# Performance work log

Measured on AMD Instinct MI355X. Metric: run time of the kernel, lower is better.

Reference implementation:

```python
import jax, jax.numpy as jnp
import numpy as np
from jax import lax

B, CIN, VS, P, E, H = 1, 1, 64, 4, 64, 8
N = (VS // P) ** 3  # 4096 patches
OUT = CIN * P ** 3  # 64
SCALE = 1.0 / float(np.sqrt(E))
EPS = 1e-5


def setup_inputs() -> dict:
    key = jax.random.key(0)
    ks = jax.random.split(key, 8)
    sc = 0.02
    return {
        "voxel": jax.random.normal(ks[0], (B, CIN, VS, VS, VS), jnp.float32),
        "conv_w": jax.random.normal(ks[1], (E, CIN, P, P, P), jnp.float32) * sc,
        "conv_b": jnp.zeros((E,), jnp.float32),
        "ln_g": jnp.ones((E,), jnp.float32),
        "ln_b": jnp.zeros((E,), jnp.float32),
        "pos_emb": jax.random.normal(ks[2], (1, N, E), jnp.float32) * sc,
        "wqk": jax.random.normal(ks[3], (E, H * E), jnp.float32) * sc,
        "bqk": jnp.zeros((H * E,), jnp.float32),
        "wv": jax.random.normal(ks[4], (E, H * E), jnp.float32) * sc,
        "bv": jnp.zeros((H * E,), jnp.float32),
        "alpha": jnp.array(1.0, jnp.float32),
        "wout": jax.random.normal(ks[5], (H * E, OUT), jnp.float32) * sc,
        "bout": jnp.zeros((OUT,), jnp.float32),
    }


def reference(voxel, conv_w, conv_b, ln_g, ln_b, pos_emb, wqk, bqk, wv, bv, alpha, wout, bout):
    # VoxelPatchEmbedding: strided Conv3d -> flatten -> permute -> LayerNorm
    emb = lax.conv_general_dilated(
        voxel, conv_w, window_strides=(P, P, P), padding="VALID",
        dimension_numbers=("NCDHW", "OIDHW", "NCDHW"))
    emb = emb + conv_b[None, :, None, None, None]
    b = emb.shape[0]
    emb = emb.reshape(b, E, -1).transpose(0, 2, 1)  # [B, N, E]
    mu = jnp.mean(emb, axis=-1, keepdims=True)
    var = jnp.var(emb, axis=-1, keepdims=True)
    emb = (emb - mu) * lax.rsqrt(var + EPS) * ln_g + ln_b
    emb = emb + pos_emb

    # tied Q/K projection; heads to dim 1: [B, H, N, E]
    qk_proj = (emb @ wqk + bqk).reshape(b, -1, H, E).transpose(0, 2, 1, 3)
    q = qk_proj
    k = qk_proj
    v = (emb @ wv + bv).reshape(b, -1, H, E).transpose(0, 2, 1, 3)

    # L2 distance: q^2 + k^2 - 2 q.k^T  -> [B, H, N, N]
    q2 = jnp.sum(q * q, axis=-1, keepdims=True)           # [B,H,N,1]
    k2 = jnp.sum(k * k, axis=-1, keepdims=True)           # [B,H,N,1]
    dist = q2 + k2.transpose(0, 1, 3, 2) - 2.0 * jnp.einsum("bhnd,bhmd->bhnm", q, k)

    scores = alpha * jnp.exp(-dist) * SCALE
    attn_w = jax.nn.softmax(scores, axis=-1)
    attn = jnp.einsum("bhnm,bhmd->bhnd", attn_w, v)       # [B,H,N,E]
    attn = attn.transpose(0, 2, 1, 3).reshape(b, -1, H * E)
    return attn @ wout + bout                              # [B, N, CIN*P^3]
```

## Files before the change

### kernel.cpp

```cpp
#include <hip/hip_runtime.h>
#include <hip/hip_bf16.h>

#define NPAT 4096
#define EDIM 64
#define NH   8
#define HE   512
#define OUTD 64

typedef short bf16x8 __attribute__((ext_vector_type(8)));
typedef float f32x4  __attribute__((ext_vector_type(4)));
typedef unsigned short u16x4 __attribute__((ext_vector_type(4)));

#if __has_builtin(__builtin_amdgcn_exp2f)
#define EXP2(x) __builtin_amdgcn_exp2f(x)
#else
#define EXP2(x) exp2f(x)
#endif

__device__ __forceinline__ ushort f2bf(float f) {
    uint u = __builtin_bit_cast(uint, f);
    return (ushort)((u + 0x7FFFu + ((u >> 16) & 1u)) >> 16);
}
__device__ __forceinline__ float bf2f(ushort b) {
    return __builtin_bit_cast(float, ((uint)b) << 16);
}

__global__ __launch_bounds__(256) void k_embed(
    const float* __restrict__ voxel,
    const float* __restrict__ conv_w,
    const float* __restrict__ conv_b,
    const float* __restrict__ ln_g, const float* __restrict__ ln_b,
    const float* __restrict__ pos,
    float* __restrict__ emb)
{
    const int b = blockIdx.x;
    const int d = b >> 6, hh = (b >> 2) & 15, wq = b & 3;
    const int t = threadIdx.x;
    __shared__ float wsm[64][68];
    __shared__ float vox[4][64];

    for (int i = t; i < 4096; i += 256) wsm[i >> 6][i & 63] = conv_w[i];
    {
        const int pair = t >> 4;
        const int q16  = t & 15;
        const float v = voxel[(d * 4 + (pair >> 2)) * 4096 + (hh * 4 + (pair & 3)) * 64 +
                              wq * 16 + q16];
        vox[q16 >> 2][pair * 4 + (q16 & 3)] = v;
    }
    __syncthreads();

    const int p = t >> 6;
    const int e = t & 63;
    const int n = d * 256 + hh * 16 + wq * 4 + p;

    float acc = conv_b[e];
    #pragma unroll
    for (int mi = 0; mi < 16; mi++) {
        const float4 vv = *(const float4*)&vox[p][mi * 4];
        const float4 ww = *(const float4*)&wsm[e][mi * 4];
        acc += vv.x * ww.x + vv.y * ww.y + vv.z * ww.z + vv.w * ww.w;
    }

    float s1 = acc, s2 = acc * acc;
    #pragma unroll
    for (int off = 1; off < 64; off <<= 1) {
        s1 += __shfl_xor(s1, off);
        s2 += __shfl_xor(s2, off);
    }
    const float mu  = s1 * (1.0f / 64.0f);
    const float var = s2 * (1.0f / 64.0f) - mu * mu;
    emb[n * 64 + e] = (acc - mu) * rsqrtf(var + 1e-5f) * ln_g[e] + ln_b[e] + pos[n * 64 + e];
}

__global__ __launch_bounds__(256) void k_wt(
    const float* __restrict__ wout,
    ushort* __restrict__ woutT)
{
    const int b = blockIdx.x;
    const int t = threadIdx.x;
    __shared__ float ld[64][65];
    for (int i = t; i < 4096; i += 256) ld[i >> 6][i & 63] = wout[(b * 64 + (i >> 6)) * 64 + (i & 63)];
    __syncthreads();
    const int o = t >> 2, kb = (t & 3) * 16;
    #pragma unroll
    for (int j = 0; j < 16; j++)
        woutT[o * 512 + b * 64 + kb + j] = f2bf(ld[kb + j][o]);
}

__global__ __launch_bounds__(256) void k_proj(
    const float* __restrict__ emb,
    const float* __restrict__ wqk, const float* __restrict__ bqk,
    const float* __restrict__ wv,  const float* __restrict__ bvv,
    ushort* __restrict__ qk_bf,
    ushort* __restrict__ vT_bf,
    float* __restrict__ q2)
{
    const int n0 = blockIdx.x * 16;
    const int h  = blockIdx.y;
    const int t  = threadIdx.x;
    const int e  = t & 63, rg = t >> 6;
    __shared__ float es[16][64];
    for (int i = t; i < 1024; i += 256) es[i >> 6][i & 63] = emb[n0 * 64 + i];
    __syncthreads();

    const int he = h * 64 + e;
    const float bq = bqk[he], bv = bvv[he];
    float aq[4] = {bq, bq, bq, bq};
    float av[4] = {bv, bv, bv, bv};

    for (int ep = 0; ep < 64; ep++) {
        const float wq = wqk[ep * HE + he];
        const float wvv = wv[ep * HE + he];
        #pragma unroll
        for (int rr = 0; rr < 4; rr++) {
            const float x = es[rg * 4 + rr][ep];
            aq[rr] += x * wq;
            av[rr] += x * wvv;
        }
    }

    u16x4 vpk;
    #pragma unroll
    for (int rr = 0; rr < 4; rr++) {
        const int n = n0 + rg * 4 + rr;
        const ushort qb = f2bf(aq[rr]);
        qk_bf[((size_t)h * NPAT + n) * 64 + e] = qb;
        const float qf = bf2f(qb);
        float s = qf * qf;
        #pragma unroll
        for (int off = 1; off < 64; off <<= 1) s += __shfl_xor(s, off);
        if (e == 0) q2[h * NPAT + n] = s;
        vpk[rr] = f2bf(av[rr]);
    }
    *(u16x4*)&vT_bf[((size_t)h * 64 + e) * NPAT + n0 + rg * 4] = vpk;
}

__global__ __launch_bounds__(1024, 8) void k_attn(
    const ushort* __restrict__ qk,
    const ushort* __restrict__ vT,
    const float* __restrict__ q2,
    const float* __restrict__ alpha,
    ushort* __restrict__ attn)
{
    const int bid = blockIdx.x;
    const int h  = bid & 7;
    const int bx = bid >> 3;
    const int tid = threadIdx.x;
    const int w  = tid >> 6;
    const int u  = w & 3;
    const int rg = w >> 2;
    const int l  = tid & 63;
    const int lr = l & 15;
    const int lg = l >> 4;
    const float L2E = 1.4426950408889634f;
    const float ccl2e = alpha[0] * 0.125f * L2E;

    __shared__ ushort kv_lds[2][2][64 * 64];
    __shared__ ushort p_lds[4][16 * 64];
    __shared__ float  zpart[4][4][16];

    const ushort* qkh = qk + (size_t)h * NPAT * 64;
    const ushort* vTh = vT + (size_t)h * 64 * NPAT;
    const float*  q2h = q2 + h * NPAT;

    const int row0 = bx * 64 + rg * 16;

    bf16x8 aq0, aq1;
    {
        const ushort* qrow = qkh + (size_t)(row0 + lr) * 64 + 8 * lg;
        aq0 = *(const bf16x8*)(qrow);
        aq1 = *(const bf16x8*)(qrow + 32);
    }
    float nq2[4];
    #pragma unroll
    for (int r = 0; r < 4; r++) nq2[r] = q2h[row0 + 4 * lg + r];

    const int w8   = w & 7;
    const int srow = w8 * 8 + (l >> 3);
    const int sch  = (l & 7) ^ (srow & 7);
    const ushort* ksrc0 = qkh + (size_t)srow * 64 + sch * 8;
    const ushort* vsrc0 = vTh + (size_t)srow * NPAT + sch * 8;
#define STAGE(bufi, it)                                                          \
    do {                                                                         \
        const ushort* _src = (w < 8) ? (ksrc0 + (size_t)(it) * 4096)             \
                                     : (vsrc0 + (size_t)(it) * 64);              \
        ushort* _dst = &kv_lds[bufi][w >> 3][w8 * 512];                          \
        __builtin_amdgcn_global_load_lds(                                        \
            (const __attribute__((address_space(1))) unsigned int*)_src,         \
            (__attribute__((address_space(3))) unsigned int*)_dst, 16, 0, 0);    \
    } while (0)

    f32x4 acc = (f32x4){0.f, 0.f, 0.f, 0.f};
    float zacc[4] = {0.f, 0.f, 0.f, 0.f};

    const int x7 = (lr & 7);
    char* prg = (char*)&p_lds[rg][0];

    STAGE(0, 0);
    float k2c = q2h[u * 16 + lr];

    for (int it = 0; it < 64; ++it) {
        const int buf = it & 1;
        __syncthreads();
        if (it + 1 < 64) STAGE(buf ^ 1, it + 1);
        float k2n = (it + 1 < 64) ? q2h[(it + 1) * 64 + u * 16 + lr] : 0.f;

        {
            const ushort* kb = &kv_lds[buf][0][0];
            const int krow = u * 16 + lr;
            bf16x8 bk0 = *(const bf16x8*)(kb + krow * 64 + ((lg ^ x7) << 3));
            bf16x8 bk1 = *(const bf16x8*)(kb + krow * 64 + (((lg + 4) ^ x7) << 3));
            f32x4 sc = (f32x4){0.f, 0.f, 0.f, 0.f};
            sc = __builtin_amdgcn_mfma_f32_16x16x32_bf16(aq0, bk0, sc, 0, 0, 0);
            sc = __builtin_amdgcn_mfma_f32_16x16x32_bf16(aq1, bk1, sc, 0, 0, 0);
            #pragma unroll
            for (int r = 0; r < 4; r++) {
                const float d = nq2[r] + k2c - 2.0f * sc[r];
                const float p = EXP2(ccl2e * EXP2(-L2E * d));
                zacc[r] += p;
                const int prow = 4 * lg + r, pcol = 16 * u + lr;
                const int byteoff = prow * 128 + ((pcol * 2) ^ ((prow & 7) << 4));
                *(ushort*)(prg + byteoff) = f2bf(p);
            }
        }
        asm volatile("s_waitcnt lgkmcnt(0)" ::: "memory");
        __builtin_amdgcn_s_barrier();

        {
            const ushort* vb = &kv_lds[buf][1][0];
            const int vrow = u * 16 + lr;
            bf16x8 bv0 = *(const bf16x8*)(vb + vrow * 64 + ((lg ^ x7) << 3));
            bf16x8 bv1 = *(const bf16x8*)(vb + vrow * 64 + (((lg + 4) ^ x7) << 3));
            char* rb = prg + lr * 128;
            const int xx = x7 << 4;
            bf16x8 pa0 = *(const bf16x8*)(rb + ((16 * lg) ^ xx));
            bf16x8 pa1 = *(const bf16x8*)(rb + ((64 + 16 * lg) ^ xx));
            acc = __builtin_amdgcn_mfma_f32_16x16x32_bf16(pa0, bv0, acc, 0, 0, 0);
            acc = __builtin_amdgcn_mfma_f32_16x16x32_bf16(pa1, bv1, acc, 0, 0, 0);
        }
        k2c = k2n;
    }
#undef STAGE

    #pragma unroll
    for (int r = 0; r < 4; r++) {
        float z = zacc[r];
        z += __shfl_xor(z, 1); z += __shfl_xor(z, 2);
        z += __shfl_xor(z, 4); z += __shfl_xor(z, 8);
        if (lr == 0) zpart[rg][u][4 * lg + r] = z;
    }
    __syncthreads();
    #pragma unroll
    for (int r = 0; r < 4; r++) {
        const int row = 4 * lg + r;
        const float zt = zpart[rg][0][row] + zpart[rg][1][row] +
                         zpart[rg][2][row] + zpart[rg][3][row];
        attn[(size_t)(row0 + row) * HE + h * 64 + u * 16 + lr] = f2bf(acc[r] / zt);
    }
}

__global__ __launch_bounds__(256) void k_out(
    const ushort* __restrict__ attn,
    const ushort* __restrict__ woutT,
    const float* __restrict__ bout,
    float* __restrict__ out)
{
    const int n0 = blockIdx.x * 8;
    const int t = threadIdx.x;
    const int w = t >> 6, l = t & 63, lr = l & 15, lg = l >> 4;
    __shared__ ushort sa[8][520];

    for (int c = t; c < 512; c += 256) {
        const int row = c >> 6, c8 = c & 63;
        *(bf16x8*)&sa[row][c8 * 8] = *(const bf16x8*)&attn[(size_t)(n0 + row) * 512 + c8 * 8];
    }
    __syncthreads();

    f32x4 acc = (f32x4){0.f, 0.f, 0.f, 0.f};
    const ushort* bp = woutT + (size_t)(w * 16 + lr) * 512 + 8 * lg;
    #pragma unroll
    for (int kk = 0; kk < 16; kk++) {
        bf16x8 a = *(const bf16x8*)&sa[lr & 7][kk * 32 + 8 * lg];
        bf16x8 bb = *(const bf16x8*)(bp + kk * 32);
        acc = __builtin_amdgcn_mfma_f32_16x16x32_bf16(a, bb, acc, 0, 0, 0);
    }
    if (lg < 2) {
        const float bo = bout[w * 16 + lr];
        #pragma unroll
        for (int r = 0; r < 4; r++)
            out[(size_t)(n0 + 4 * lg + r) * 64 + w * 16 + lr] = acc[r] + bo;
    }
}

extern "C" void kernel_launch(void* const* d_in, const int* in_sizes, int n_in,
                              void* d_out, int out_size, void* d_ws, size_t ws_size,
                              hipStream_t stream) {
    (void)in_sizes; (void)n_in; (void)out_size; (void)ws_size;
    const float* voxel  = (const float*)d_in[0];
    const float* conv_w = (const float*)d_in[1];
    const float* conv_b = (const float*)d_in[2];
    const float* ln_g   = (const float*)d_in[3];
    const float* ln_b   = (const float*)d_in[4];
    const float* pos    = (const float*)d_in[5];
    const float* wqk    = (const float*)d_in[6];
    const float* bqk    = (const float*)d_in[7];
    const float* wv     = (const float*)d_in[8];
    const float* bvv    = (const float*)d_in[9];
    const float* alpha  = (const float*)d_in[10];
    const float* wout   = (const float*)d_in[11];
    const float* bout   = (const float*)d_in[12];
    float* out = (float*)d_out;

    char* ws = (char*)d_ws;
    float*  emb     = (float*) (ws);
    ushort* qk_bf   = (ushort*)(ws + (1u << 20));
    ushort* vT_bf   = (ushort*)(ws + 5u * (1u << 20));
    float*  q2      = (float*) (ws + 9u * (1u << 20));
    ushort* attn_bf = (ushort*)(ws + 9u * (1u << 20) + (128u << 10));
    ushort* woutT   = (ushort*)(ws + 13u * (1u << 20) + (128u << 10));

    k_embed<<<1024, 256, 0, stream>>>(voxel, conv_w, conv_b, ln_g, ln_b, pos, emb);
    k_wt<<<8, 256, 0, stream>>>(wout, woutT);
    k_proj<<<dim3(NPAT / 16, NH), 256, 0, stream>>>(emb, wqk, bqk, wv, bvv, qk_bf, vT_bf, q2);
    k_attn<<<NPAT / 64 * NH, 1024, 0, stream>>>(qk_bf, vT_bf, q2, alpha, attn_bf);
    k_out<<<NPAT / 8, 256, 0, stream>>>(attn_bf, woutT, bout, out);
}
```

Baseline: 202.1 us.

## Fuse embed, weight transpose and projection; triple-buffer attention K/V staging

Merges the patch-embedding conv+LayerNorm, the output-weight transpose and the QK/V projection into one launch. Each projection block now recomputes the embedding for its 16 patches, so the fp32 emb buffer is never written out or read back. The attention kernel moves from double to triple buffering of K/V tiles in LDS, with vmcnt-based waits in place of a full sync each iteration. It also preloads all per-head k2 norms into shared memory instead of reading them from global each step. The cost is that the conv and LayerNorm work is repeated once per head (8x) and LDS use per attention block goes up.

Result: slower. 220.1 us (+8.9%).

```diff
diff --git a/kernel.cpp b/kernel.cpp
--- a/kernel.cpp
+++ b/kernel.cpp
@@ -25,82 +25,77 @@
     return __builtin_bit_cast(float, ((uint)b) << 16);
 }
 
-__global__ __launch_bounds__(256) void k_embed(
-    const float* __restrict__ voxel,
-    const float* __restrict__ conv_w,
-    const float* __restrict__ conv_b,
-    const float* __restrict__ ln_g, const float* __restrict__ ln_b,
-    const float* __restrict__ pos,
-    float* __restrict__ emb)
+__global__ __launch_bounds__(256) void k_embproj(
+    const float* __restrict__ voxel, const float* __restrict__ conv_w,
+    const float* __restrict__ conv_b, const float* __restrict__ ln_g,
+    const float* __restrict__ ln_b, const float* __restrict__ pos,
+    const float* __restrict__ wqk, const float* __restrict__ bqk,
+    const float* __restrict__ wv, const float* __restrict__ bvv,
+    const float* __restrict__ wout,
+    ushort* __restrict__ qk_bf,
+    ushort* __restrict__ vT_bf,
+    float* __restrict__ q2,
+    ushort* __restrict__ woutT)
 {
-    const int b = blockIdx.x;
-    const int d = b >> 6, hh = (b >> 2) & 15, wq = b & 3;
+    __shared__ float smem[64 * 65 + 16 * 64 + 16 * 64];
+    float (*wsm)[65] = (float(*)[65])smem;
+    float (*vox)[64] = (float(*)[64])(smem + 64 * 65);
+    float (*es)[64]  = (float(*)[64])(smem + 64 * 65 + 16 * 64);
     const int t = threadIdx.x;
-    __shared__ float wsm[64][68];
-    __shared__ float vox[4][64];
+
+    if (blockIdx.y == 8) {
+        if (blockIdx.x >= 8) return;
+        const int b = blockIdx.x;
+        for (int i = t; i < 4096; i += 256)
+            wsm[i >> 6][i & 63] = wout[(b * 64 + (i >> 6)) * 64 + (i & 63)];
+        __syncthreads();
+        const int o = t >> 2, kb = (t & 3) * 16;
+        #pragma unroll
+        for (int j = 0; j < 16; j++)
+            woutT[o * 512 + b * 64 + kb + j] = f2bf(wsm[kb + j][o]);
+        return;
+    }
+
+    const int bx = blockIdx.x, h = blockIdx.y;
+    const int n0 = bx * 16;
+    const int d = bx >> 4, hh = bx & 15;
+    const int e = t & 63, rg = t >> 6;
 
     for (int i = t; i < 4096; i += 256) wsm[i >> 6][i & 63] = conv_w[i];
     {
         const int pair = t >> 4;
-        const int q16  = t & 15;
-        const float v = voxel[(d * 4 + (pair >> 2)) * 4096 + (hh * 4 + (pair & 3)) * 64 +
-                              wq * 16 + q16];
-        vox[q16 >> 2][pair * 4 + (q16 & 3)] = v;
-    }
-    __syncthreads();
-
-    const int p = t >> 6;
-    const int e = t & 63;
-    const int n = d * 256 + hh * 16 + wq * 4 + p;
-
-    float acc = conv_b[e];
-    #pragma unroll
-    for (int mi = 0; mi < 16; mi++) {
-        const float4 vv = *(const float4*)&vox[p][mi * 4];
-        const float4 ww = *(const float4*)&wsm[e][mi * 4];
-        acc += vv.x * ww.x + vv.y * ww.y + vv.z * ww.z + vv.w * ww.w;
-    }
-
-    float s1 = acc, s2 = acc * acc;
-    #pragma unroll
-    for (int off = 1; off < 64; off <<= 1) {
-        s1 += __shfl_xor(s1, off);
-        s2 += __shfl_xor(s2, off);
-    }
-    const float mu  = s1 * (1.0f / 64.0f);
-    const float var = s2 * (1.0f / 64.0f) - mu * mu;
-    emb[n * 64 + e] = (acc - mu) * rsqrtf(var + 1e-5f) * ln_g[e] + ln_b[e] + pos[n * 64 + e];
-}
-
-__global__ __launch_bounds__(256) void k_wt(
-    const float* __restrict__ wout,
-    ushort* __restrict__ woutT)
-{
-    const int b = blockIdx.x;
-    const int t = threadIdx.x;
-    __shared__ float ld[64][65];
-    for (int i = t; i < 4096; i += 256) ld[i >> 6][i & 63] = wout[(b * 64 + (i >> 6)) * 64 + (i & 63)];
-    __syncthreads();
-    const int o = t >> 2, kb = (t & 3) * 16;
-    #pragma unroll
-    for (int j = 0; j < 16; j++)
-        woutT[o * 512 + b * 64 + kb + j] = f2bf(ld[kb + j][o]);
-}
-
-__global__ __launch_bounds__(256) void k_proj(
-    const float* __restrict__ emb,
-    const float* __restrict__ wqk, const float* __restrict__ bqk,
-    const float* __restrict__ wv,  const float* __restrict__ bvv,
-    ushort* __restrict__ qk_bf,
-    ushort* __restrict__ vT_bf,
-    float* __restrict__ q2)
-{
-    const int n0 = blockIdx.x * 16;
-    const int h  = blockIdx.y;
-    const int t  = threadIdx.x;
-    const int e  = t & 63, rg = t >> 6;
-    __shared__ float es[16][64];
-    for (int i = t; i < 1024; i += 256) es[i >> 6][i & 63] = emb[n0 * 64 + i];
+        const int off4 = (t & 15) * 4;
+        const float4 v = *(const float4*)&voxel[(d * 4 + (pair >> 2)) * 4096 +
+                                                (hh * 4 + (pair & 3)) * 64 + off4];
+        *(float4*)&vox[pair][off4] = v;
+    }
+    __syncthreads();
+
+    {
+        float acc[4];
+        #pragma unroll
+        for (int rr = 0; rr < 4; rr++) acc[rr] = conv_b[e];
+        for (int m = 0; m < 64; m++) {
+            const float wm = wsm[e][m];
+            #pragma unroll
+            for (int rr = 0; rr < 4; rr++)
+                acc[rr] += vox[m >> 2][(rg * 4 + rr) * 4 + (m & 3)] * wm;
+        }
+        #pragma unroll
+        for (int rr = 0; rr < 4; rr++) {
+            const int row = rg * 4 + rr;
+            float s1 = acc[rr], s2 = acc[rr] * acc[rr];
+            #pragma unroll
+            for (int off = 1; off < 64; off <<= 1) {
+                s1 += __shfl_xor(s1, off);
+                s2 += __shfl_xor(s2, off);
+            }
+            const float mu  = s1 * (1.0f / 64.0f);
+            const float var = s2 * (1.0f / 64.0f) - mu * mu;
+            es[row][e] = (acc[rr] - mu) * rsqrtf(var + 1e-5f) * ln_g[e] + ln_b[e] +
+                         pos[(n0 + row) * 64 + e];
+        }
+    }
     __syncthreads();
 
     const int he = h * 64 + e;
@@ -109,7 +104,7 @@
     float av[4] = {bv, bv, bv, bv};
 
     for (int ep = 0; ep < 64; ep++) {
-        const float wq = wqk[ep * HE + he];
+        const float wq  = wqk[ep * HE + he];
         const float wvv = wv[ep * HE + he];
         #pragma unroll
         for (int rr = 0; rr < 4; rr++) {
@@ -155,9 +150,10 @@
     const float L2E = 1.4426950408889634f;
     const float ccl2e = alpha[0] * 0.125f * L2E;
 
-    __shared__ ushort kv_lds[2][2][64 * 64];
+    __shared__ ushort kv_lds[3][2][64 * 64];
     __shared__ ushort p_lds[4][16 * 64];
     __shared__ float  zpart[4][4][16];
+    __shared__ float  q2s[4096];
 
     const ushort* qkh = qk + (size_t)h * NPAT * 64;
     const ushort* vTh = vT + (size_t)h * 64 * NPAT;
@@ -174,6 +170,8 @@
     float nq2[4];
     #pragma unroll
     for (int r = 0; r < 4; r++) nq2[r] = q2h[row0 + 4 * lg + r];
+
+    *(float4*)&q2s[tid * 4] = *(const float4*)&q2h[tid * 4];
 
     const int w8   = w & 7;
     const int srow = w8 * 8 + (l >> 3);
@@ -197,13 +195,19 @@
     char* prg = (char*)&p_lds[rg][0];
 
     STAGE(0, 0);
-    float k2c = q2h[u * 16 + lr];
-
+    STAGE(1, 1);
+    __syncthreads();
+
+    int buf = 0;
     for (int it = 0; it < 64; ++it) {
-        const int buf = it & 1;
-        __syncthreads();
-        if (it + 1 < 64) STAGE(buf ^ 1, it + 1);
-        float k2n = (it + 1 < 64) ? q2h[(it + 1) * 64 + u * 16 + lr] : 0.f;
+        if (it == 63) { asm volatile("s_waitcnt vmcnt(0)" ::: "memory"); }
+        else         { asm volatile("s_waitcnt vmcnt(1)" ::: "memory"); }
+        __builtin_amdgcn_s_barrier();
+        if (it + 2 < 64) {
+            int b2 = buf + 2; if (b2 >= 3) b2 -= 3;
+            STAGE(b2, it + 2);
+        }
+        const float k2c = q2s[it * 64 + u * 16 + lr];
 
         {
             const ushort* kb = &kv_lds[buf][0][0];
@@ -238,7 +242,7 @@
             acc = __builtin_amdgcn_mfma_f32_16x16x32_bf16(pa0, bv0, acc, 0, 0, 0);
             acc = __builtin_amdgcn_mfma_f32_16x16x32_bf16(pa1, bv1, acc, 0, 0, 0);
         }
-        k2c = k2n;
+        buf = (buf == 2) ? 0 : buf + 1;
     }
 #undef STAGE
 
@@ -312,16 +316,15 @@
     float* out = (float*)d_out;
 
     char* ws = (char*)d_ws;
-    float*  emb     = (float*) (ws);
     ushort* qk_bf   = (ushort*)(ws + (1u << 20));
     ushort* vT_bf   = (ushort*)(ws + 5u * (1u << 20));
     float*  q2      = (float*) (ws + 9u * (1u << 20));
     ushort* attn_bf = (ushort*)(ws + 9u * (1u << 20) + (128u << 10));
     ushort* woutT   = (ushort*)(ws + 13u * (1u << 20) + (128u << 10));
 
-    k_embed<<<1024, 256, 0, stream>>>(voxel, conv_w, conv_b, ln_g, ln_b, pos, emb);
-    k_wt<<<8, 256, 0, stream>>>(wout, woutT);
-    k_proj<<<dim3(NPAT / 16, NH), 256, 0, stream>>>(emb, wqk, bqk, wv, bvv, qk_bf, vT_bf, q2);
+    k_embproj<<<dim3(NPAT / 16, NH + 1), 256, 0, stream>>>(
+        voxel, conv_w, conv_b, ln_g, ln_b, pos, wqk, bqk, wv, bvv, wout,
+        qk_bf, vT_bf, q2, woutT);
     k_attn<<<NPAT / 64 * NH, 1024, 0, stream>>>(qk_bf, vT_bf, q2, alpha, attn_bf);
     k_out<<<NPAT / 8, 256, 0, stream>>>(attn_bf, woutT, bout, out);
 }
```
